# Performance work log

Measured on AMD Instinct MI355X. Metric: run time of the kernel, lower is better.

The kernel has to match this reference:

```python
import jax, jax.numpy as jnp
import numpy as np

B, S, M = 128, 4096, 20
LOG_2PI = float(np.log(2.0 * np.pi))


def setup_inputs() -> dict:
    key = jax.random.key(0)
    k1, k2, k3, k4, k5 = jax.random.split(key, 5)
    xs = jax.random.normal(k1, (B, S, 5), dtype=jnp.float32)
    logits_pred = jax.random.normal(k2, (B, S, M), dtype=jnp.float32)
    mus_pred = jax.random.normal(k3, (B, S, M, 2), dtype=jnp.float32)
    # sigmas are Cholesky entries (l00, l10, l11); diagonal must be positive.
    sigmas_pred = jax.random.uniform(k4, (B, S, M, 3), dtype=jnp.float32) + 0.1
    pen_pred = jax.random.uniform(k5, (B, S, 3), dtype=jnp.float32)
    return {"xs": xs, "logits_pred": logits_pred, "mus_pred": mus_pred,
            "sigmas_pred": sigmas_pred, "pen_pred": pen_pred}


def reference(xs, logits_pred, mus_pred, sigmas_pred, pen_pred):
    # split stroke-5 format: (dx_abs, dy_abs) + 3 pen states
    position_true = xs[..., :2]          # [B,S,2]
    pen_true = xs[..., 2:]               # [B,S,3]

    # relative positions: roll by 1 along seq, first step prev = (0,0)
    position_prev = jnp.concatenate(
        [jnp.zeros_like(position_true[:, :1]), position_true[:, :-1]], axis=1)
    rel = position_true - position_prev  # [B,S,2]

    # closed-form 2D Gaussian log-density with lower-tri Cholesky
    # scale_tril entries (tril_indices(2,2) order): l00, l10, l11
    l00 = sigmas_pred[..., 0]            # [B,S,M]
    l10 = sigmas_pred[..., 1]
    l11 = sigmas_pred[..., 2]
    d = rel[:, :, None, :] - mus_pred    # [B,S,M,2]
    z0 = d[..., 0] / l00
    z1 = (d[..., 1] - l10 * z0) / l11
    comp_logp = (-0.5 * (z0 * z0 + z1 * z1)
                 - LOG_2PI - jnp.log(l00) - jnp.log(l11))  # [B,S,M]

    # mixture log-prob via logsumexp over components
    mix_logp = jax.nn.logsumexp(
        jax.nn.log_softmax(logits_pred, axis=-1) + comp_logp, axis=-1)  # [B,S]
    position_loss = -jnp.sum(mix_logp)

    # pen loss: faithful to source -> CrossEntropyLoss(input=pen_true, target=pen_pred)
    # (soft-target CE, mean reduction over B*S rows)
    logp = jax.nn.log_softmax(pen_true.reshape(-1, 3), axis=-1)
    pen_loss = jnp.mean(-jnp.sum(pen_pred.reshape(-1, 3) * logp, axis=-1))

    return position_loss + pen_loss
```

## Files before the change

### kernel.cpp

```cpp
#include <hip/hip_runtime.h>
#include <math.h>

#define BB 128
#define SS 4096
#define MM 20
#define NPOS (BB * SS)
#define BLOCK 256
#define NBLOCKS (NPOS / BLOCK)

__device__ __forceinline__ float fast_rcp(float x) { return __builtin_amdgcn_rcpf(x); }

__global__ __launch_bounds__(BLOCK) void sketch_main(
    const float* __restrict__ xs,
    const float* __restrict__ logits,
    const float* __restrict__ mus,
    const float* __restrict__ sigmas,
    const float* __restrict__ pen_pred,
    float* __restrict__ partials)
{
    const float LOG_2PI = 1.8378770664093453f;
    const int idx = blockIdx.x * BLOCK + threadIdx.x;
    const int s = idx & (SS - 1);

    const float* xp = xs + (size_t)idx * 5;
    float px = xp[0], py = xp[1];
    float pt0 = xp[2], pt1 = xp[3], pt2 = xp[4];
    float qx = 0.0f, qy = 0.0f;
    if (s != 0) { qx = xp[-5]; qy = xp[-4]; }
    const float rx = px - qx, ry = py - qy;

    const float4* sp = (const float4*)(sigmas + (size_t)idx * 60);
    const float4* mp = (const float4*)(mus    + (size_t)idx * 40);
    const float4* lp = (const float4*)(logits + (size_t)idx * 20);

    float mx_a = -INFINITY;
    float se_a = 0.0f;
    float se_l = 0.0f;

#pragma unroll
    for (int g = 0; g < 5; ++g) {
        float4 s0 = sp[3*g+0], s1 = sp[3*g+1], s2 = sp[3*g+2];
        float4 m0 = mp[2*g+0], m1 = mp[2*g+1];
        float4 lg4 = lp[g];

        float sv[12] = { s0.x, s0.y, s0.z, s0.w, s1.x, s1.y,
                         s1.z, s1.w, s2.x, s2.y, s2.z, s2.w };
        float mv[8]  = { m0.x, m0.y, m0.z, m0.w, m1.x, m1.y, m1.z, m1.w };
        float lv[4]  = { lg4.x, lg4.y, lg4.z, lg4.w };

#pragma unroll
        for (int c = 0; c < 4; ++c) {
            float l00 = sv[3*c], l10 = sv[3*c+1], l11 = sv[3*c+2];
            float z0 = (rx - mv[2*c]) * fast_rcp(l00);
            float z1 = ((ry - mv[2*c+1]) - l10 * z0) * fast_rcp(l11);
            float av = lv[c] - 0.5f * (z0*z0 + z1*z1) - LOG_2PI - __logf(l00 * l11);
            float nm = fmaxf(mx_a, av);
            se_a = se_a * __expf(mx_a - nm) + __expf(av - nm);
            mx_a = nm;
            se_l += __expf(lv[c]);
        }
    }

    float mix_logp = (mx_a + __logf(se_a)) - __logf(se_l);

    float pm = fmaxf(pt0, fmaxf(pt1, pt2));
    float lse3 = pm + __logf(__expf(pt0 - pm) + __expf(pt1 - pm) + __expf(pt2 - pm));
    const float* pp = pen_pred + (size_t)idx * 3;
    float pen = -(pp[0] * (pt0 - lse3) + pp[1] * (pt1 - lse3) + pp[2] * (pt2 - lse3));

    float val = -mix_logp + pen * (1.0f / (float)NPOS);

#pragma unroll
    for (int off = 32; off > 0; off >>= 1) val += __shfl_down(val, off, 64);
    __shared__ float red[BLOCK / 64];
    int lane = threadIdx.x & 63, wid = threadIdx.x >> 6;
    if (lane == 0) red[wid] = val;
    __syncthreads();
    if (threadIdx.x == 0)
        partials[blockIdx.x] = red[0] + red[1] + red[2] + red[3];
}

__global__ __launch_bounds__(BLOCK) void sketch_reduce(
    const float* __restrict__ partials, float* __restrict__ out)
{
    float v = 0.0f;
    for (int i = threadIdx.x; i < NBLOCKS; i += BLOCK) v += partials[i];
#pragma unroll
    for (int off = 32; off > 0; off >>= 1) v += __shfl_down(v, off, 64);
    __shared__ float red[BLOCK / 64];
    int lane = threadIdx.x & 63, wid = threadIdx.x >> 6;
    if (lane == 0) red[wid] = v;
    __syncthreads();
    if (threadIdx.x == 0)
        out[0] = red[0] + red[1] + red[2] + red[3];
}

extern "C" void kernel_launch(void* const* d_in, const int* in_sizes, int n_in,
                              void* d_out, int out_size, void* d_ws, size_t ws_size,
                              hipStream_t stream) {
    const float* xs       = (const float*)d_in[0];
    const float* logits   = (const float*)d_in[1];
    const float* mus      = (const float*)d_in[2];
    const float* sigmas   = (const float*)d_in[3];
    const float* pen_pred = (const float*)d_in[4];
    float* out = (float*)d_out;
    float* partials = (float*)d_ws;

    sketch_main<<<NBLOCKS, BLOCK, 0, stream>>>(xs, logits, mus, sigmas, pen_pred, partials);
    sketch_reduce<<<1, BLOCK, 0, stream>>>(partials, out);
}
```

Before: 309.8 us.

## Stage mixture params through LDS with coalesced loads and split components across wave halves

Each block now cooperatively loads the sigmas, mus and logits for 64 positions into shared memory using contiguous float4 loads, replacing per-thread strided 240-byte reads. The 20 mixture components per position are then split between two waves (12 and 8 components), and the partial logsumexp states are merged through shared memory. The aim is better global-load coalescing and more parallelism per position. The cost is extra barriers, LDS traffic with strided float4 reads that may bank-conflict, and an uneven split of work between the two waves.

After: 309.4 us. About the same (-0.1%).

```diff
diff --git a/kernel.cpp b/kernel.cpp
--- a/kernel.cpp
+++ b/kernel.cpp
@@ -5,10 +5,37 @@
 #define SS 4096
 #define MM 20
 #define NPOS (BB * SS)
-#define BLOCK 256
-#define NBLOCKS (NPOS / BLOCK)
+#define BLOCK 128
+#define HALF 64
+#define TILE 128
+#define NBLOCKS (NPOS / TILE)
 
 __device__ __forceinline__ float fast_rcp(float x) { return __builtin_amdgcn_rcpf(x); }
+
+__device__ __forceinline__ void comp_group4(
+    const float4* __restrict__ bS4, const float4* __restrict__ bM4,
+    const float4* __restrict__ bL4, int g, float rx, float ry,
+    float& mx, float& se, float& sel)
+{
+    const float LOG_2PI = 1.8378770664093453f;
+    float4 s0 = bS4[3*g], s1 = bS4[3*g+1], s2 = bS4[3*g+2];
+    float4 m0 = bM4[2*g], m1 = bM4[2*g+1];
+    float4 l4 = bL4[g];
+    float sv[12] = { s0.x,s0.y,s0.z,s0.w, s1.x,s1.y,s1.z,s1.w, s2.x,s2.y,s2.z,s2.w };
+    float mv[8]  = { m0.x,m0.y,m0.z,m0.w, m1.x,m1.y,m1.z,m1.w };
+    float lv[4]  = { l4.x,l4.y,l4.z,l4.w };
+#pragma unroll
+    for (int c = 0; c < 4; ++c) {
+        float l00 = sv[3*c], l10 = sv[3*c+1], l11 = sv[3*c+2];
+        float z0 = (rx - mv[2*c]) * fast_rcp(l00);
+        float z1 = ((ry - mv[2*c+1]) - l10 * z0) * fast_rcp(l11);
+        float av = lv[c] - 0.5f * (z0*z0 + z1*z1) - LOG_2PI - __logf(l00 * l11);
+        float nm = fmaxf(mx, av);
+        se = se * __expf(mx - nm) + __expf(av - nm);
+        mx = nm;
+        sel += __expf(lv[c]);
+    }
+}
 
 __global__ __launch_bounds__(BLOCK) void sketch_main(
     const float* __restrict__ xs,
@@ -18,76 +45,85 @@
     const float* __restrict__ pen_pred,
     float* __restrict__ partials)
 {
-    const float LOG_2PI = 1.8378770664093453f;
-    const int idx = blockIdx.x * BLOCK + threadIdx.x;
-    const int s = idx & (SS - 1);
+    __shared__ float4 sS[HALF * 15];
+    __shared__ float4 sM[HALF * 10];
+    __shared__ float4 sL[HALF * 5];
+    __shared__ float  cmb[HALF * 3];
+    __shared__ float  red[2];
 
-    const float* xp = xs + (size_t)idx * 5;
-    float px = xp[0], py = xp[1];
-    float pt0 = xp[2], pt1 = xp[3], pt2 = xp[4];
-    float qx = 0.0f, qy = 0.0f;
-    if (s != 0) { qx = xp[-5]; qy = xp[-4]; }
-    const float rx = px - qx, ry = py - qy;
+    const int tid  = threadIdx.x;
+    const int lpos = tid & (HALF - 1);
+    const int hi   = tid >> 6;
+    float acc = 0.0f;
 
-    const float4* sp = (const float4*)(sigmas + (size_t)idx * 60);
-    const float4* mp = (const float4*)(mus    + (size_t)idx * 40);
-    const float4* lp = (const float4*)(logits + (size_t)idx * 20);
+    for (int h = 0; h < 2; ++h) {
+        const int base = blockIdx.x * TILE + h * HALF;
 
-    float mx_a = -INFINITY;
-    float se_a = 0.0f;
-    float se_l = 0.0f;
+        const float4* gS = (const float4*)(sigmas + (size_t)base * 60);
+        for (int i = tid; i < HALF * 15; i += BLOCK) sS[i] = gS[i];
+        const float4* gM = (const float4*)(mus + (size_t)base * 40);
+        for (int i = tid; i < HALF * 10; i += BLOCK) sM[i] = gM[i];
+        const float4* gL = (const float4*)(logits + (size_t)base * 20);
+        for (int i = tid; i < HALF * 5; i += BLOCK) sL[i] = gL[i];
+        __syncthreads();
+
+        const int p = base + lpos;
+        const int s = p & (SS - 1);
+        const float* xp = xs + (size_t)p * 5;
+        float rx = xp[0], ry = xp[1];
+        if (s != 0) { rx -= xp[-5]; ry -= xp[-4]; }
+
+        const float4* bS4 = sS + lpos * 15;
+        const float4* bM4 = sM + lpos * 10;
+        const float4* bL4 = sL + lpos * 5;
+
+        float mx = -INFINITY, se = 0.0f, sel = 0.0f;
+        if (hi == 0) {
+            comp_group4(bS4, bM4, bL4, 0, rx, ry, mx, se, sel);
+            comp_group4(bS4, bM4, bL4, 1, rx, ry, mx, se, sel);
+            comp_group4(bS4, bM4, bL4, 2, rx, ry, mx, se, sel);
+        } else {
+            comp_group4(bS4, bM4, bL4, 3, rx, ry, mx, se, sel);
+            comp_group4(bS4, bM4, bL4, 4, rx, ry, mx, se, sel);
+        }
+
+        if (hi == 1) {
+            cmb[3*lpos+0] = mx; cmb[3*lpos+1] = se; cmb[3*lpos+2] = sel;
+        }
+        __syncthreads();
+        if (hi == 0) {
+            float m2 = cmb[3*lpos+0], s2 = cmb[3*lpos+1], l2 = cmb[3*lpos+2];
+            float m = fmaxf(mx, m2);
+            float se_a = se * __expf(mx - m) + s2 * __expf(m2 - m);
+            float se_l = sel + l2;
+            float mix_logp = (m + __logf(se_a)) - __logf(se_l);
+
+            float pt0 = xp[2], pt1 = xp[3], pt2 = xp[4];
+            float pm = fmaxf(pt0, fmaxf(pt1, pt2));
+            float lse3 = pm + __logf(__expf(pt0-pm) + __expf(pt1-pm) + __expf(pt2-pm));
+            const float* pp = pen_pred + (size_t)p * 3;
+            float pen = -(pp[0]*(pt0-lse3) + pp[1]*(pt1-lse3) + pp[2]*(pt2-lse3));
+
+            acc += -mix_logp + pen * (1.0f / (float)NPOS);
+        }
+        __syncthreads();
+    }
 
 #pragma unroll
-    for (int g = 0; g < 5; ++g) {
-        float4 s0 = sp[3*g+0], s1 = sp[3*g+1], s2 = sp[3*g+2];
-        float4 m0 = mp[2*g+0], m1 = mp[2*g+1];
-        float4 lg4 = lp[g];
-
-        float sv[12] = { s0.x, s0.y, s0.z, s0.w, s1.x, s1.y,
-                         s1.z, s1.w, s2.x, s2.y, s2.z, s2.w };
-        float mv[8]  = { m0.x, m0.y, m0.z, m0.w, m1.x, m1.y, m1.z, m1.w };
-        float lv[4]  = { lg4.x, lg4.y, lg4.z, lg4.w };
-
-#pragma unroll
-        for (int c = 0; c < 4; ++c) {
-            float l00 = sv[3*c], l10 = sv[3*c+1], l11 = sv[3*c+2];
-            float z0 = (rx - mv[2*c]) * fast_rcp(l00);
-            float z1 = ((ry - mv[2*c+1]) - l10 * z0) * fast_rcp(l11);
-            float av = lv[c] - 0.5f * (z0*z0 + z1*z1) - LOG_2PI - __logf(l00 * l11);
-            float nm = fmaxf(mx_a, av);
-            se_a = se_a * __expf(mx_a - nm) + __expf(av - nm);
-            mx_a = nm;
-            se_l += __expf(lv[c]);
-        }
-    }
-
-    float mix_logp = (mx_a + __logf(se_a)) - __logf(se_l);
-
-    float pm = fmaxf(pt0, fmaxf(pt1, pt2));
-    float lse3 = pm + __logf(__expf(pt0 - pm) + __expf(pt1 - pm) + __expf(pt2 - pm));
-    const float* pp = pen_pred + (size_t)idx * 3;
-    float pen = -(pp[0] * (pt0 - lse3) + pp[1] * (pt1 - lse3) + pp[2] * (pt2 - lse3));
-
-    float val = -mix_logp + pen * (1.0f / (float)NPOS);
-
-#pragma unroll
-    for (int off = 32; off > 0; off >>= 1) val += __shfl_down(val, off, 64);
-    __shared__ float red[BLOCK / 64];
-    int lane = threadIdx.x & 63, wid = threadIdx.x >> 6;
-    if (lane == 0) red[wid] = val;
+    for (int off = 32; off > 0; off >>= 1) acc += __shfl_down(acc, off, 64);
+    if ((tid & 63) == 0) red[tid >> 6] = acc;
     __syncthreads();
-    if (threadIdx.x == 0)
-        partials[blockIdx.x] = red[0] + red[1] + red[2] + red[3];
+    if (tid == 0) partials[blockIdx.x] = red[0] + red[1];
 }
 
-__global__ __launch_bounds__(BLOCK) void sketch_reduce(
+__global__ __launch_bounds__(256) void sketch_reduce(
     const float* __restrict__ partials, float* __restrict__ out)
 {
     float v = 0.0f;
-    for (int i = threadIdx.x; i < NBLOCKS; i += BLOCK) v += partials[i];
+    for (int i = threadIdx.x; i < NBLOCKS; i += 256) v += partials[i];
 #pragma unroll
     for (int off = 32; off > 0; off >>= 1) v += __shfl_down(v, off, 64);
-    __shared__ float red[BLOCK / 64];
+    __shared__ float red[4];
     int lane = threadIdx.x & 63, wid = threadIdx.x >> 6;
     if (lane == 0) red[wid] = v;
     __syncthreads();
@@ -107,5 +143,5 @@
     float* partials = (float*)d_ws;
 
     sketch_main<<<NBLOCKS, BLOCK, 0, stream>>>(xs, logits, mus, sigmas, pen_pred, partials);
-    sketch_reduce<<<1, BLOCK, 0, stream>>>(partials, out);
+    sketch_reduce<<<1, 256, 0, stream>>>(partials, out);
 }
```

## Grid-stride two positions per thread with software-pipelined loads and two-pass logsumexp

Applied to the files above, without the earlier changes.

Shrinks the grid from 2048 to 1024 blocks, so each thread processes two positions strided by the grid size. Loads are double-buffered across the five 4-component groups, and the online logsumexp becomes a two-pass max-then-sum over a 20-entry array. The aim is more memory-level parallelism, a shorter serial exp dependency chain and fewer partials for the final reduce. The cost is higher register pressure, which may lower occupancy on this memory-bound kernel.

Result: faster. 287.6 us (-7.2%).

```diff
diff --git a/kernel.cpp b/kernel.cpp
--- a/kernel.cpp
+++ b/kernel.cpp
@@ -6,9 +6,82 @@
 #define MM 20
 #define NPOS (BB * SS)
 #define BLOCK 256
-#define NBLOCKS (NPOS / BLOCK)
+#define GRID 1024
+#define STRIDE (BLOCK * GRID)
+#define PITER (NPOS / STRIDE)
 
 __device__ __forceinline__ float fast_rcp(float x) { return __builtin_amdgcn_rcpf(x); }
+
+__device__ __forceinline__ void group4(
+    float4 s0, float4 s1, float4 s2, float4 m0, float4 m1, float4 l4,
+    float rx, float ry, float* a , float& sel)
+{
+    const float LOG_2PI = 1.8378770664093453f;
+    float sv[12] = {s0.x,s0.y,s0.z,s0.w, s1.x,s1.y,s1.z,s1.w, s2.x,s2.y,s2.z,s2.w};
+    float mv[8]  = {m0.x,m0.y,m0.z,m0.w, m1.x,m1.y,m1.z,m1.w};
+    float lv[4]  = {l4.x,l4.y,l4.z,l4.w};
+#pragma unroll
+    for (int c = 0; c < 4; ++c) {
+        float l00 = sv[3*c], l10 = sv[3*c+1], l11 = sv[3*c+2];
+        float z0 = (rx - mv[2*c]) * fast_rcp(l00);
+        float z1 = ((ry - mv[2*c+1]) - l10 * z0) * fast_rcp(l11);
+        a[c] = lv[c] - 0.5f * (z0*z0 + z1*z1) - LOG_2PI - __logf(l00 * l11);
+        sel += __expf(lv[c]);
+    }
+}
+
+__device__ __forceinline__ float position_nll(
+    const float* __restrict__ xs, const float* __restrict__ logits,
+    const float* __restrict__ mus, const float* __restrict__ sigmas,
+    const float* __restrict__ pen_pred, int p)
+{
+    const int s = p & (SS - 1);
+    const float* xp = xs + (size_t)p * 5;
+    float rx = xp[0], ry = xp[1];
+    if (s != 0) { rx -= xp[-5]; ry -= xp[-4]; }
+
+    const float4* sp = (const float4*)(sigmas + (size_t)p * 60);
+    const float4* mp = (const float4*)(mus    + (size_t)p * 40);
+    const float4* lp = (const float4*)(logits + (size_t)p * 20);
+
+    float a[20];
+    float sel = 0.0f;
+
+    float4 As0 = sp[0],  As1 = sp[1],  As2 = sp[2];
+    float4 Am0 = mp[0],  Am1 = mp[1];
+    float4 Al  = lp[0];
+    float4 Bs0 = sp[3],  Bs1 = sp[4],  Bs2 = sp[5];
+    float4 Bm0 = mp[2],  Bm1 = mp[3];
+    float4 Bl  = lp[1];
+
+    group4(As0, As1, As2, Am0, Am1, Al, rx, ry, a + 0, sel);
+    As0 = sp[6];  As1 = sp[7];  As2 = sp[8];
+    Am0 = mp[4];  Am1 = mp[5];  Al = lp[2];
+    group4(Bs0, Bs1, Bs2, Bm0, Bm1, Bl, rx, ry, a + 4, sel);
+    Bs0 = sp[9];  Bs1 = sp[10]; Bs2 = sp[11];
+    Bm0 = mp[6];  Bm1 = mp[7];  Bl = lp[3];
+    group4(As0, As1, As2, Am0, Am1, Al, rx, ry, a + 8, sel);
+    As0 = sp[12]; As1 = sp[13]; As2 = sp[14];
+    Am0 = mp[8];  Am1 = mp[9];  Al = lp[4];
+    group4(Bs0, Bs1, Bs2, Bm0, Bm1, Bl, rx, ry, a + 12, sel);
+    group4(As0, As1, As2, Am0, Am1, Al, rx, ry, a + 16, sel);
+
+    float mx = a[0];
+#pragma unroll
+    for (int c = 1; c < MM; ++c) mx = fmaxf(mx, a[c]);
+    float se = 0.0f;
+#pragma unroll
+    for (int c = 0; c < MM; ++c) se += __expf(a[c] - mx);
+    float mix_logp = (mx + __logf(se)) - __logf(sel);
+
+    float pt0 = xp[2], pt1 = xp[3], pt2 = xp[4];
+    float pm = fmaxf(pt0, fmaxf(pt1, pt2));
+    float lse3 = pm + __logf(__expf(pt0 - pm) + __expf(pt1 - pm) + __expf(pt2 - pm));
+    const float* pp = pen_pred + (size_t)p * 3;
+    float pen = -(pp[0] * (pt0 - lse3) + pp[1] * (pt1 - lse3) + pp[2] * (pt2 - lse3));
+
+    return -mix_logp + pen * (1.0f / (float)NPOS);
+}
 
 __global__ __launch_bounds__(BLOCK) void sketch_main(
     const float* __restrict__ xs,
@@ -18,76 +91,29 @@
     const float* __restrict__ pen_pred,
     float* __restrict__ partials)
 {
-    const float LOG_2PI = 1.8378770664093453f;
-    const int idx = blockIdx.x * BLOCK + threadIdx.x;
-    const int s = idx & (SS - 1);
+    const int tid = blockIdx.x * BLOCK + threadIdx.x;
 
-    const float* xp = xs + (size_t)idx * 5;
-    float px = xp[0], py = xp[1];
-    float pt0 = xp[2], pt1 = xp[3], pt2 = xp[4];
-    float qx = 0.0f, qy = 0.0f;
-    if (s != 0) { qx = xp[-5]; qy = xp[-4]; }
-    const float rx = px - qx, ry = py - qy;
-
-    const float4* sp = (const float4*)(sigmas + (size_t)idx * 60);
-    const float4* mp = (const float4*)(mus    + (size_t)idx * 40);
-    const float4* lp = (const float4*)(logits + (size_t)idx * 20);
-
-    float mx_a = -INFINITY;
-    float se_a = 0.0f;
-    float se_l = 0.0f;
+    float acc = position_nll(xs, logits, mus, sigmas, pen_pred, tid);
+    acc      += position_nll(xs, logits, mus, sigmas, pen_pred, tid + STRIDE);
 
 #pragma unroll
-    for (int g = 0; g < 5; ++g) {
-        float4 s0 = sp[3*g+0], s1 = sp[3*g+1], s2 = sp[3*g+2];
-        float4 m0 = mp[2*g+0], m1 = mp[2*g+1];
-        float4 lg4 = lp[g];
-
-        float sv[12] = { s0.x, s0.y, s0.z, s0.w, s1.x, s1.y,
-                         s1.z, s1.w, s2.x, s2.y, s2.z, s2.w };
-        float mv[8]  = { m0.x, m0.y, m0.z, m0.w, m1.x, m1.y, m1.z, m1.w };
-        float lv[4]  = { lg4.x, lg4.y, lg4.z, lg4.w };
-
-#pragma unroll
-        for (int c = 0; c < 4; ++c) {
-            float l00 = sv[3*c], l10 = sv[3*c+1], l11 = sv[3*c+2];
-            float z0 = (rx - mv[2*c]) * fast_rcp(l00);
-            float z1 = ((ry - mv[2*c+1]) - l10 * z0) * fast_rcp(l11);
-            float av = lv[c] - 0.5f * (z0*z0 + z1*z1) - LOG_2PI - __logf(l00 * l11);
-            float nm = fmaxf(mx_a, av);
-            se_a = se_a * __expf(mx_a - nm) + __expf(av - nm);
-            mx_a = nm;
-            se_l += __expf(lv[c]);
-        }
-    }
-
-    float mix_logp = (mx_a + __logf(se_a)) - __logf(se_l);
-
-    float pm = fmaxf(pt0, fmaxf(pt1, pt2));
-    float lse3 = pm + __logf(__expf(pt0 - pm) + __expf(pt1 - pm) + __expf(pt2 - pm));
-    const float* pp = pen_pred + (size_t)idx * 3;
-    float pen = -(pp[0] * (pt0 - lse3) + pp[1] * (pt1 - lse3) + pp[2] * (pt2 - lse3));
-
-    float val = -mix_logp + pen * (1.0f / (float)NPOS);
-
-#pragma unroll
-    for (int off = 32; off > 0; off >>= 1) val += __shfl_down(val, off, 64);
+    for (int off = 32; off > 0; off >>= 1) acc += __shfl_down(acc, off, 64);
     __shared__ float red[BLOCK / 64];
     int lane = threadIdx.x & 63, wid = threadIdx.x >> 6;
-    if (lane == 0) red[wid] = val;
+    if (lane == 0) red[wid] = acc;
     __syncthreads();
     if (threadIdx.x == 0)
         partials[blockIdx.x] = red[0] + red[1] + red[2] + red[3];
 }
 
-__global__ __launch_bounds__(BLOCK) void sketch_reduce(
+__global__ __launch_bounds__(256) void sketch_reduce(
     const float* __restrict__ partials, float* __restrict__ out)
 {
     float v = 0.0f;
-    for (int i = threadIdx.x; i < NBLOCKS; i += BLOCK) v += partials[i];
+    for (int i = threadIdx.x; i < GRID; i += 256) v += partials[i];
 #pragma unroll
     for (int off = 32; off > 0; off >>= 1) v += __shfl_down(v, off, 64);
-    __shared__ float red[BLOCK / 64];
+    __shared__ float red[4];
     int lane = threadIdx.x & 63, wid = threadIdx.x >> 6;
     if (lane == 0) red[wid] = v;
     __syncthreads();
@@ -106,6 +132,6 @@
     float* out = (float*)d_out;
     float* partials = (float*)d_ws;
 
-    sketch_main<<<NBLOCKS, BLOCK, 0, stream>>>(xs, logits, mus, sigmas, pen_pred, partials);
-    sketch_reduce<<<1, BLOCK, 0, stream>>>(partials, out);
+    sketch_main<<<GRID, BLOCK, 0, stream>>>(xs, logits, mus, sigmas, pen_pred, partials);
+    sketch_reduce<<<1, 256, 0, stream>>>(partials, out);
 }
```
